# Kernel tuning notes

Hardware: AMD Instinct MI355X
Metric: run time of the kernel (lower is better)

## Reference

```python
import jax, jax.numpy as jnp
import numpy as np

NUM_HEADS = 16
HEAD_DIM = 64
HIDDEN = NUM_HEADS * HEAD_DIM  # 1024
SEQ_LEN = 4096


def setup_inputs() -> dict:
    key = jax.random.key(0)
    ks = jax.random.split(key, 8)
    hidden_states = jax.random.normal(ks[0], (SEQ_LEN, HIDDEN), dtype=jnp.float32)
    cu_seqlens = jnp.sort(jax.random.randint(ks[1], (5,), 0, SEQ_LEN)).astype(jnp.int32)
    cos = jax.random.uniform(ks[2], (SEQ_LEN, HEAD_DIM), dtype=jnp.float32)
    sin = jax.random.uniform(ks[3], (SEQ_LEN, HEAD_DIM), dtype=jnp.float32)
    W_qkv = jax.random.normal(ks[4], (HIDDEN, 3 * HIDDEN), dtype=jnp.float32) * 0.02
    b_qkv = jax.random.normal(ks[5], (3 * HIDDEN,), dtype=jnp.float32) * 0.02
    W_proj = jax.random.normal(ks[6], (HIDDEN, HIDDEN), dtype=jnp.float32) * 0.02
    b_proj = jax.random.normal(ks[7], (HIDDEN,), dtype=jnp.float32) * 0.02
    return {
        "hidden_states": hidden_states,
        "cu_seqlens": cu_seqlens,
        "cos": cos,
        "sin": sin,
        "W_qkv": W_qkv,
        "b_qkv": b_qkv,
        "W_proj": W_proj,
        "b_proj": b_proj,
    }


def _rotate_half(x):
    x1, x2 = jnp.split(x, 2, axis=-1)
    return jnp.concatenate([-x2, x1], axis=-1)


def reference(hidden_states, cu_seqlens, cos, sin, W_qkv, b_qkv, W_proj, b_proj):
    # NOTE: original module does not use cu_seqlens for masking (full dense attention).
    seq_len = hidden_states.shape[0]
    qkv = hidden_states @ W_qkv + b_qkv  # (S, 3*H)
    qkv = qkv.reshape(seq_len, 3, NUM_HEADS, HEAD_DIM)
    q, k, v = qkv[:, 0], qkv[:, 1], qkv[:, 2]  # (S, nh, hd)
    c = cos[:, None, :]
    s = sin[:, None, :]
    q = q * c + _rotate_half(q) * s
    k = k * c + _rotate_half(k) * s
    scale = 1.0 / jnp.sqrt(jnp.float32(HEAD_DIM))
    # (nh, S, hd)
    q = q.transpose(1, 0, 2)
    k = k.transpose(1, 0, 2)
    v = v.transpose(1, 0, 2)
    attn = jnp.einsum('hqd,hkd->hqk', q, k) * scale
    attn = jax.nn.softmax(attn, axis=-1)
    out = jnp.einsum('hqk,hkd->hqd', attn, v)
    out = out.transpose(1, 0, 2).reshape(seq_len, HIDDEN)
    return out @ W_proj + b_proj
```

## Files before the change

kernel.cpp:

```cpp
#include <hip/hip_runtime.h>
#include <type_traits>

typedef short bf16x8 __attribute__((ext_vector_type(8)));
typedef float f32x4  __attribute__((ext_vector_type(4)));
typedef unsigned short u16;

#define MFMA(a,b,c) __builtin_amdgcn_mfma_f32_16x16x32_bf16((a),(b),(c),0,0,0)

__device__ __forceinline__ float bf2f(u16 u){ unsigned x=((unsigned)u)<<16; return __builtin_bit_cast(float,x); }
__device__ __forceinline__ u16 f2bf(float f){ unsigned x=__builtin_bit_cast(unsigned,f); x += 0x7fffu + ((x>>16)&1u); return (u16)(x>>16); }

#if __has_builtin(__builtin_amdgcn_cvt_pk_bf16_f32)
typedef __bf16 hwbf2 __attribute__((ext_vector_type(2)));
__device__ __forceinline__ unsigned pkbf(float a, float b){
  hwbf2 r = __builtin_amdgcn_cvt_pk_bf16_f32(a, b);
  return __builtin_bit_cast(unsigned, r);
}
#else
__device__ __forceinline__ unsigned pkbf(float a, float b){
  unsigned ua = __builtin_bit_cast(unsigned, a), ub = __builtin_bit_cast(unsigned, b);
  ua += 0x7fffu + ((ua>>16)&1u);
  ub += 0x7fffu + ((ub>>16)&1u);
  return __builtin_amdgcn_perm(ub, ua, 0x07060302u);
}
#endif

#if __has_builtin(__builtin_amdgcn_exp2f)
#define EXP2(x) __builtin_amdgcn_exp2f(x)
#else
#define EXP2(x) exp2f(x)
#endif

__device__ __forceinline__ void async_cp16(const u16* g, u16* l){
  __builtin_amdgcn_global_load_lds((const __attribute__((address_space(1))) void*)g,
                                   (__attribute__((address_space(3))) void*)l, 16, 0, 0);
}

__global__ __launch_bounds__(256) void prep(
    const float* __restrict__ H, const float* __restrict__ Wqkv, const float* __restrict__ Wproj,
    u16* __restrict__ Hb, u16* __restrict__ WqkvT, u16* __restrict__ WprojT)
{
  __shared__ u16 tile[32][33];
  const int bid = blockIdx.x, tid = threadIdx.x;
  if (bid < 4096) {
    int i = (bid*256 + tid)*4;
    float4 v = *(const float4*)(H + i);
    ushort4 o;
    o.x = f2bf(v.x); o.y = f2bf(v.y); o.z = f2bf(v.z); o.w = f2bf(v.w);
    *(ushort4*)(Hb + i) = o;
    return;
  }
  const float* in; u16* out; int R, C, bx, by;
  if (bid < 7168) { int t = bid-4096; in=Wqkv; out=WqkvT; R=1024; C=3072; bx=t%96; by=t/96; }
  else            { int t = bid-7168; in=Wproj; out=WprojT; R=1024; C=1024; bx=t%32; by=t/32; }
  int bc = bx*32, br = by*32;
  int tx = tid & 31, ty = tid >> 5;
  #pragma unroll
  for (int i=ty;i<32;i+=8) tile[i][tx] = f2bf(in[(size_t)(br+i)*C + bc + tx]);
  __syncthreads();
  #pragma unroll
  for (int i=ty;i<32;i+=8) out[(size_t)(bc+i)*R + br + tx] = tile[tx][i];
}

__global__ __launch_bounds__(256) void gemm_qkv_rope(
    const u16* __restrict__ A, const u16* __restrict__ Bt,
    const float* __restrict__ bias, const float* __restrict__ cosb, const float* __restrict__ sinb,
    u16* __restrict__ Qo, u16* __restrict__ Ko, u16* __restrict__ Vt)
{
  constexpr int K = 1024;
  __shared__ __align__(16) u16 smem[128*128];
  u16* const As = smem;
  u16* const Bs = smem + 128*64;
  const int m0 = blockIdx.y*128, n0 = blockIdx.x*128;
  const int tid = threadIdx.x, wave = tid>>6, lane = tid&63;
  const int wr = (wave>>1)*64, wc = (wave&1)*64;
  const int ml = lane&15, quad = lane>>4;
  const int lrow8 = lane>>3, lchk = lane&7;
  const int swzg = (lchk ^ lrow8)*8;
  const u16* gA[4]; u16* lA[4];
  const u16* gB[4]; u16* lB[4];
  #pragma unroll
  for (int t=0;t<4;t++){
    gA[t] = A  + (size_t)(m0 + wave*32 + t*8 + lrow8)*K + swzg;
    lA[t] = &As[(wave*32 + t*8)*64];
    gB[t] = Bt + (size_t)(n0 + wave*32 + t*8 + lrow8)*K + swzg;
    lB[t] = &Bs[(wave*32 + t*8)*64];
  }
  f32x4 acc[4][4] = {};
  const int rch0 = ( quad     ^ (ml&7))*8;
  const int rch1 = ((quad|4) ^ (ml&7))*8;
  for (int k0=0; k0<K; k0+=64) {
    #pragma unroll
    for (int t=0;t<4;t++){ async_cp16(gA[t]+k0, lA[t]); async_cp16(gB[t]+k0, lB[t]); }
    __syncthreads();
    #pragma unroll
    for (int kk=0;kk<2;kk++){
      const int rc = kk ? rch1 : rch0;
      bf16x8 af[4], bfr[4];
      #pragma unroll
      for (int i=0;i<4;i++)  af[i]  = *(const bf16x8*)&As[(wr+i*16+ml)*64 + rc];
      #pragma unroll
      for (int j=0;j<4;j++) bfr[j] = *(const bf16x8*)&Bs[(wc+j*16+ml)*64 + rc];
      #pragma unroll
      for (int i=0;i<4;i++)
        #pragma unroll
        for (int j=0;j<4;j++)
          acc[i][j] = MFMA(af[i], bfr[j], acc[i][j]);
    }
    __syncthreads();
  }
  const int region = n0 >> 10;
  if (region == 2) {
    #pragma unroll
    for (int j=0;j<4;j++){
      int d2 = wc + j*16 + ml;
      float bv = bias[n0 + d2];
      #pragma unroll
      for (int i=0;i<4;i++){
        int t0 = wr + i*16 + quad*4;
        #pragma unroll
        for (int r=0;r<4;r++){
          int t = t0 + r;
          int c = (d2 >> 3) ^ (t & 15);
          smem[t*128 + c*8 + (d2 & 7)] = f2bf(acc[i][j][r] + bv);
        }
      }
    }
    __syncthreads();
    const int hbase = (n0 - 2048) >> 6;
    const int pc  = (tid & 15) * 8;
    const int rid = tid >> 4;
    const int tq  = pc >> 5;
    #pragma unroll
    for (int it=0; it<8; it++){
      int d2 = rid + it*16;
      int hh = hbase + (d2 >> 6);
      int dd = d2 & 63;
      union { uint4 u; ushort s[8]; } w;
      #pragma unroll
      for (int pp=0; pp<8; pp++){
        int p = pc + pp;
        int tlog = ((p>>2)&1)*16 + ((p>>3)&3)*4 + (p&3);
        int t_src = tq*32 + tlog;
        int cc = (d2 >> 3) ^ (t_src & 15);
        w.s[pp] = smem[t_src*128 + cc*8 + (d2 & 7)];
      }
      *(uint4*)&Vt[((size_t)hh*64 + dd)*4096 + m0 + pc] = w.u;
    }
  } else {
    u16* dst = region ? Ko : Qo;
    const float qs = region ? 1.0f : 0.125f*1.44269504f;
    #pragma unroll
    for (int j=0;j<4;j++){
      int col = n0 + wc + j*16 + ml;
      int dloc = col & 63, hh = (col & 1023) >> 6;
      float bv  = bias[col];
      float bvp = bias[col ^ 32];
      float sgn = (dloc < 32) ? -1.f : 1.f;
      #pragma unroll
      for (int i=0;i<4;i++){
        int row0 = m0 + wr + i*16 + quad*4;
        #pragma unroll
        for (int r=0;r<4;r++){
          int t = row0 + r;
          float c = cosb[t*64 + dloc], s = sinb[t*64 + dloc];
          float val = acc[i][j][r]   + bv;
          float par = acc[i][j^2][r] + bvp;
          dst[((size_t)hh*4096 + t)*64 + dloc] = f2bf((val*c + sgn*par*s)*qs);
        }
      }
    }
  }
}

template<int BN, typename OutT>
__global__ __launch_bounds__(256) void gemm_bt_bias(
    const u16* __restrict__ A, const u16* __restrict__ Bt,
    const float* __restrict__ bias, OutT* __restrict__ C,
    int M, int N, int K)
{
  __shared__ __align__(16) u16 As[128*64];
  __shared__ __align__(16) u16 Bs[BN*64];
  const int m0 = blockIdx.y*128, n0 = blockIdx.x*BN;
  const int tid = threadIdx.x, wave = tid>>6, lane = tid&63;
  const int wr = (wave>>1)*64, wc = (wave&1)*(BN/2);
  const int ml = lane&15, quad = lane>>4;
  const int lrow8 = lane>>3, lchk = lane&7;
  const int swzg = (lchk ^ lrow8)*8;
  const u16* gA[4]; u16* lA[4];
  #pragma unroll
  for (int t=0;t<4;t++){
    gA[t] = A + (size_t)(m0 + wave*32 + t*8 + lrow8)*K + swzg;
    lA[t] = &As[(wave*32 + t*8)*64];
  }
  constexpr int BI = BN/32;
  const u16* gB[BI]; u16* lB[BI];
  #pragma unroll
  for (int t=0;t<BI;t++){
    gB[t] = Bt + (size_t)(n0 + wave*(BN/4) + t*8 + lrow8)*K + swzg;
    lB[t] = &Bs[(wave*(BN/4) + t*8)*64];
  }
  constexpr int NJ = BN/32;
  f32x4 acc[4][NJ] = {};
  const int rch0 = ( quad     ^ (ml&7))*8;
  const int rch1 = ((quad|4) ^ (ml&7))*8;
  for (int k0=0; k0<K; k0+=64) {
    #pragma unroll
    for (int t=0;t<4;t++)  async_cp16(gA[t]+k0, lA[t]);
    #pragma unroll
    for (int t=0;t<BI;t++) async_cp16(gB[t]+k0, lB[t]);
    __syncthreads();
    #pragma unroll
    for (int kk=0;kk<2;kk++){
      const int rc = kk ? rch1 : rch0;
      bf16x8 af[4], bfr[NJ];
      #pragma unroll
      for (int i=0;i<4;i++)  af[i]  = *(const bf16x8*)&As[(wr+i*16+ml)*64 + rc];
      #pragma unroll
      for (int j=0;j<NJ;j++) bfr[j] = *(const bf16x8*)&Bs[(wc+j*16+ml)*64 + rc];
      #pragma unroll
      for (int i=0;i<4;i++)
        #pragma unroll
        for (int j=0;j<NJ;j++)
          acc[i][j] = MFMA(af[i], bfr[j], acc[i][j]);
    }
    __syncthreads();
  }
  #pragma unroll
  for (int j=0;j<NJ;j++){
    int col = n0 + wc + j*16 + ml;
    float bv = bias[col];
    #pragma unroll
    for (int i=0;i<4;i++){
      int row0 = m0 + wr + i*16 + quad*4;
      #pragma unroll
      for (int r=0;r<4;r++){
        float val = acc[i][j][r] + bv;
        if constexpr (std::is_same_v<OutT, float>)
          C[(size_t)(row0+r)*N + col] = val;
        else
          C[(size_t)(row0+r)*N + col] = f2bf(val);
      }
    }
  }
}

__global__ __launch_bounds__(256,4) void flash_attn(
    const u16* __restrict__ Q, const u16* __restrict__ Kg, const u16* __restrict__ VT,
    u16* __restrict__ O0, u16* __restrict__ O1, float* __restrict__ Lpart)
{
  constexpr int SEQ=4096, HALF=2048;
  __shared__ __align__(16) u16 Ks[64*64];
  __shared__ __align__(16) u16 Vs[64*64];
  const int lin = blockIdx.x;
  const int idx = (lin & 7)*128 + (lin >> 3);
  const int qt = idx & 31, h = (idx >> 5) & 15, ks = idx >> 9;
  const int tid=threadIdx.x, wave=tid>>6, lane=tid&63;
  const int ml=lane&15, quad=lane>>4;
  const int qbase = qt*128 + wave*32;
  bf16x8 qf[2][2];
  #pragma unroll
  for (int qi=0; qi<2; qi++){
    const u16* qp = Q + ((size_t)h*SEQ + qbase + qi*16 + ml)*64;
    qf[qi][0] = *(const bf16x8*)(qp + quad*8);
    qf[qi][1] = *(const bf16x8*)(qp + 32 + quad*8);
  }
  const bf16x8 ones = {0x3F80,0x3F80,0x3F80,0x3F80,0x3F80,0x3F80,0x3F80,0x3F80};
  f32x4 o[2][4] = {};
  f32x4 accsum[2] = {};
  const int lrow8 = lane>>3, lchk = lane&7;
  const int swzg = (lchk ^ lrow8)*8;
  const u16* kgl = Kg + (size_t)h*SEQ*64 + (size_t)(ks*HALF + wave*16 + lrow8)*64 + swzg;
  const u16* vgl = VT + (size_t)h*64*SEQ + (size_t)(wave*16 + lrow8)*SEQ + ks*HALF + swzg;
  u16* kl0 = &Ks[(wave*16  )*64];
  u16* kl1 = &Ks[(wave*16+8)*64];
  u16* vl0 = &Vs[(wave*16  )*64];
  u16* vl1 = &Vs[(wave*16+8)*64];
  const int swzA = ( quad     ^ (ml&7))*8;
  const int swzB = ((quad^4) ^ (ml&7))*8;

  for (int k0=0;k0<HALF;k0+=64) {
    async_cp16(kgl + (size_t)k0*64,       kl0);
    async_cp16(kgl + (size_t)k0*64 + 512, kl1);
    async_cp16(vgl + k0,                  vl0);
    async_cp16(vgl + 8*SEQ + k0,          vl1);
    __syncthreads();
    f32x4 s[2][4];
    #pragma unroll
    for (int kb=0;kb<4;kb++){
      bf16x8 kf0 = *(const bf16x8*)&Ks[(kb*16+ml)*64 + swzA];
      bf16x8 kf1 = *(const bf16x8*)&Ks[(kb*16+ml)*64 + swzB];
      f32x4 z0={0,0,0,0}, z1={0,0,0,0};
      z0 = MFMA(kf0, qf[0][0], z0); s[0][kb] = MFMA(kf1, qf[0][1], z0);
      z1 = MFMA(kf0, qf[1][0], z1); s[1][kb] = MFMA(kf1, qf[1][1], z1);
    }
    bf16x8 vf[4][2];
    #pragma unroll
    for (int db=0;db<4;db++){
      vf[db][0] = *(const bf16x8*)&Vs[(db*16+ml)*64 + swzA];
      vf[db][1] = *(const bf16x8*)&Vs[(db*16+ml)*64 + swzB];
    }
    #pragma unroll
    for (int qi=0; qi<2; qi++)
      #pragma unroll
      for (int p=0;p<2;p++){
        float e0 = EXP2(s[qi][2*p][0]),   e1 = EXP2(s[qi][2*p][1]);
        float e2 = EXP2(s[qi][2*p][2]),   e3 = EXP2(s[qi][2*p][3]);
        float e4 = EXP2(s[qi][2*p+1][0]), e5 = EXP2(s[qi][2*p+1][1]);
        float e6 = EXP2(s[qi][2*p+1][2]), e7 = EXP2(s[qi][2*p+1][3]);
        union { uint4 u; bf16x8 v; } pf;
        pf.u.x = pkbf(e0,e1); pf.u.y = pkbf(e2,e3);
        pf.u.z = pkbf(e4,e5); pf.u.w = pkbf(e6,e7);
        accsum[qi] = MFMA(ones, pf.v, accsum[qi]);
        #pragma unroll
        for (int db=0;db<4;db++)
          o[qi][db] = MFMA(vf[db][p], pf.v, o[qi][db]);
      }
    __syncthreads();
  }
  u16* op = ks ? O1 : O0;
  #pragma unroll
  for (int qi=0;qi<2;qi++){
    size_t rb = (size_t)(qbase + qi*16 + ml)*1024 + h*64;
    #pragma unroll
    for (int db=0;db<4;db++){
      uint2 w;
      w.x = pkbf(o[qi][db][0], o[qi][db][1]);
      w.y = pkbf(o[qi][db][2], o[qi][db][3]);
      *(uint2*)&op[rb + db*16 + quad*4] = w;
    }
  }
  if (quad==0){
    float* lp = Lpart + (size_t)ks*65536 + (size_t)h*4096 + qbase;
    lp[ml]    = accsum[0][0];
    lp[16+ml] = accsum[1][0];
  }
}

__global__ __launch_bounds__(256) void combine_softmax2(
    const u16* __restrict__ O0, const u16* __restrict__ O1,
    const float* __restrict__ L, u16* __restrict__ AO)
{
  int i = (blockIdx.x*256 + threadIdx.x)*4;
  int row = i >> 10, col = i & 1023, h = col >> 6;
  int li = h*4096 + row;
  float inv = 1.f/(L[li] + L[li+65536]);
  ushort4 a = *(const ushort4*)(O0+i);
  ushort4 b = *(const ushort4*)(O1+i);
  ushort4 o;
  o.x = f2bf((bf2f(a.x)+bf2f(b.x))*inv);
  o.y = f2bf((bf2f(a.y)+bf2f(b.y))*inv);
  o.z = f2bf((bf2f(a.z)+bf2f(b.z))*inv);
  o.w = f2bf((bf2f(a.w)+bf2f(b.w))*inv);
  *(ushort4*)(AO+i) = o;
}

extern "C" void kernel_launch(void* const* d_in, const int* in_sizes, int n_in,
                              void* d_out, int out_size, void* d_ws, size_t ws_size,
                              hipStream_t stream)
{
  (void)in_sizes; (void)n_in; (void)out_size; (void)ws_size;
  const float* H     = (const float*)d_in[0];
  const float* cosb  = (const float*)d_in[2];
  const float* sinb  = (const float*)d_in[3];
  const float* Wqkv  = (const float*)d_in[4];
  const float* bqkv  = (const float*)d_in[5];
  const float* Wproj = (const float*)d_in[6];
  const float* bproj = (const float*)d_in[7];
  float* out = (float*)d_out;
  char* ws = (char*)d_ws;
  float* Lpart  = (float*)(ws + 0);
  u16*   WprojT = (u16*)(ws + 2097152);
  u16*   Hb     = (u16*)(ws + 4194304);
  u16*   Opart0 = (u16*)(ws + 4194304);
  u16*   Qb     = (u16*)(ws + 12582912);
  u16*   AO     = (u16*)(ws + 12582912);
  u16*   Kb     = (u16*)(ws + 20971520);
  u16*   VTb    = (u16*)(ws + 29360128);
  u16*   WqkvT  = (u16*)(ws + 37748736);
  u16*   Opart1 = (u16*)(ws + 44040192);

  hipLaunchKernelGGL(prep, dim3(8192), dim3(256), 0, stream, H, Wqkv, Wproj, Hb, WqkvT, WprojT);
  hipLaunchKernelGGL(gemm_qkv_rope, dim3(24,32), dim3(256), 0, stream,
                     Hb, WqkvT, bqkv, cosb, sinb, Qb, Kb, VTb);
  hipLaunchKernelGGL(flash_attn, dim3(1024), dim3(256), 0, stream, Qb, Kb, VTb,
                     Opart0, Opart1, Lpart);
  hipLaunchKernelGGL(combine_softmax2, dim3(4096), dim3(256), 0, stream,
                     Opart0, Opart1, Lpart, AO);
  hipLaunchKernelGGL((gemm_bt_bias<64,float>), dim3(16,32), dim3(256), 0, stream,
                     AO, WprojT, bproj, out, 4096, 1024, 1024);
}
```

Baseline: 237.5 us.

## Fuse split-K softmax combine into output projection GEMM

Removes the separate combine kernel and the AO intermediate buffer. The projection GEMM now loads both partial attention outputs and accumulates MFMAs over each. Because each 64-wide K tile is exactly one head, it scales the per-tile partial sum by the per-row inverse softmax denominator from shared memory. This saves one launch and a full read/write pass of the attention output, but doubles A-tile loads and MFMAs in the projection GEMM and adds LDS use.

Measured after the change: 239.9 us. Within noise of the previous version (+1.0%).

```diff
diff --git a/kernel.cpp b/kernel.cpp
--- a/kernel.cpp
+++ b/kernel.cpp
@@ -168,78 +168,6 @@
           float par = acc[i][j^2][r] + bvp;
           dst[((size_t)hh*4096 + t)*64 + dloc] = f2bf((val*c + sgn*par*s)*qs);
         }
-      }
-    }
-  }
-}
-
-template<int BN, typename OutT>
-__global__ __launch_bounds__(256) void gemm_bt_bias(
-    const u16* __restrict__ A, const u16* __restrict__ Bt,
-    const float* __restrict__ bias, OutT* __restrict__ C,
-    int M, int N, int K)
-{
-  __shared__ __align__(16) u16 As[128*64];
-  __shared__ __align__(16) u16 Bs[BN*64];
-  const int m0 = blockIdx.y*128, n0 = blockIdx.x*BN;
-  const int tid = threadIdx.x, wave = tid>>6, lane = tid&63;
-  const int wr = (wave>>1)*64, wc = (wave&1)*(BN/2);
-  const int ml = lane&15, quad = lane>>4;
-  const int lrow8 = lane>>3, lchk = lane&7;
-  const int swzg = (lchk ^ lrow8)*8;
-  const u16* gA[4]; u16* lA[4];
-  #pragma unroll
-  for (int t=0;t<4;t++){
-    gA[t] = A + (size_t)(m0 + wave*32 + t*8 + lrow8)*K + swzg;
-    lA[t] = &As[(wave*32 + t*8)*64];
-  }
-  constexpr int BI = BN/32;
-  const u16* gB[BI]; u16* lB[BI];
-  #pragma unroll
-  for (int t=0;t<BI;t++){
-    gB[t] = Bt + (size_t)(n0 + wave*(BN/4) + t*8 + lrow8)*K + swzg;
-    lB[t] = &Bs[(wave*(BN/4) + t*8)*64];
-  }
-  constexpr int NJ = BN/32;
-  f32x4 acc[4][NJ] = {};
-  const int rch0 = ( quad     ^ (ml&7))*8;
-  const int rch1 = ((quad|4) ^ (ml&7))*8;
-  for (int k0=0; k0<K; k0+=64) {
-    #pragma unroll
-    for (int t=0;t<4;t++)  async_cp16(gA[t]+k0, lA[t]);
-    #pragma unroll
-    for (int t=0;t<BI;t++) async_cp16(gB[t]+k0, lB[t]);
-    __syncthreads();
-    #pragma unroll
-    for (int kk=0;kk<2;kk++){
-      const int rc = kk ? rch1 : rch0;
-      bf16x8 af[4], bfr[NJ];
-      #pragma unroll
-      for (int i=0;i<4;i++)  af[i]  = *(const bf16x8*)&As[(wr+i*16+ml)*64 + rc];
-      #pragma unroll
-      for (int j=0;j<NJ;j++) bfr[j] = *(const bf16x8*)&Bs[(wc+j*16+ml)*64 + rc];
-      #pragma unroll
-      for (int i=0;i<4;i++)
-        #pragma unroll
-        for (int j=0;j<NJ;j++)
-          acc[i][j] = MFMA(af[i], bfr[j], acc[i][j]);
-    }
-    __syncthreads();
-  }
-  #pragma unroll
-  for (int j=0;j<NJ;j++){
-    int col = n0 + wc + j*16 + ml;
-    float bv = bias[col];
-    #pragma unroll
-    for (int i=0;i<4;i++){
-      int row0 = m0 + wr + i*16 + quad*4;
-      #pragma unroll
-      for (int r=0;r<4;r++){
-        float val = acc[i][j][r] + bv;
-        if constexpr (std::is_same_v<OutT, float>)
-          C[(size_t)(row0+r)*N + col] = val;
-        else
-          C[(size_t)(row0+r)*N + col] = f2bf(val);
       }
     }
   }
@@ -337,22 +265,97 @@
   }
 }
 
-__global__ __launch_bounds__(256) void combine_softmax2(
-    const u16* __restrict__ O0, const u16* __restrict__ O1,
-    const float* __restrict__ L, u16* __restrict__ AO)
-{
-  int i = (blockIdx.x*256 + threadIdx.x)*4;
-  int row = i >> 10, col = i & 1023, h = col >> 6;
-  int li = h*4096 + row;
-  float inv = 1.f/(L[li] + L[li+65536]);
-  ushort4 a = *(const ushort4*)(O0+i);
-  ushort4 b = *(const ushort4*)(O1+i);
-  ushort4 o;
-  o.x = f2bf((bf2f(a.x)+bf2f(b.x))*inv);
-  o.y = f2bf((bf2f(a.y)+bf2f(b.y))*inv);
-  o.z = f2bf((bf2f(a.z)+bf2f(b.z))*inv);
-  o.w = f2bf((bf2f(a.w)+bf2f(b.w))*inv);
-  *(ushort4*)(AO+i) = o;
+__global__ __launch_bounds__(256) void gemm_proj_combine(
+    const u16* __restrict__ O0, const u16* __restrict__ O1, const float* __restrict__ L,
+    const u16* __restrict__ Bt, const float* __restrict__ bias, float* __restrict__ C)
+{
+  constexpr int N = 1024, K = 1024;
+  __shared__ __align__(16) u16 As[128*64];
+  __shared__ __align__(16) u16 A1s[128*64];
+  __shared__ __align__(16) u16 Bs[64*64];
+  __shared__ float invL[16*128];
+  const int m0 = blockIdx.y*128, n0 = blockIdx.x*64;
+  const int tid = threadIdx.x, wave = tid>>6, lane = tid&63;
+  const int wr = (wave>>1)*64, wc = (wave&1)*32;
+  const int ml = lane&15, quad = lane>>4;
+  const int lrow8 = lane>>3, lchk = lane&7;
+  const int swzg = (lchk ^ lrow8)*8;
+  #pragma unroll
+  for (int e = tid; e < 2048; e += 256){
+    int hh = e >> 7, t = e & 127;
+    int li = hh*4096 + m0 + t;
+    invL[e] = 1.0f/(L[li] + L[li + 65536]);
+  }
+  const u16* gA0[4]; u16* lA0[4];
+  const u16* gA1[4]; u16* lA1[4];
+  #pragma unroll
+  for (int t=0;t<4;t++){
+    gA0[t] = O0 + (size_t)(m0 + wave*32 + t*8 + lrow8)*K + swzg;
+    lA0[t] = &As[(wave*32 + t*8)*64];
+    gA1[t] = O1 + (size_t)(m0 + wave*32 + t*8 + lrow8)*K + swzg;
+    lA1[t] = &A1s[(wave*32 + t*8)*64];
+  }
+  const u16* gB[2]; u16* lB[2];
+  #pragma unroll
+  for (int t=0;t<2;t++){
+    gB[t] = Bt + (size_t)(n0 + wave*16 + t*8 + lrow8)*K + swzg;
+    lB[t] = &Bs[(wave*16 + t*8)*64];
+  }
+  f32x4 acc[4][2] = {};
+  const int rch0 = ( quad     ^ (ml&7))*8;
+  const int rch1 = ((quad|4) ^ (ml&7))*8;
+  for (int k0=0; k0<K; k0+=64) {
+    #pragma unroll
+    for (int t=0;t<4;t++){ async_cp16(gA0[t]+k0, lA0[t]); async_cp16(gA1[t]+k0, lA1[t]); }
+    #pragma unroll
+    for (int t=0;t<2;t++)  async_cp16(gB[t]+k0, lB[t]);
+    __syncthreads();
+    f32x4 acch[4][2] = {};
+    #pragma unroll
+    for (int kk=0;kk<2;kk++){
+      const int rc = kk ? rch1 : rch0;
+      bf16x8 af0[4], af1[4], bfr[2];
+      #pragma unroll
+      for (int i=0;i<4;i++){
+        af0[i] = *(const bf16x8*)&As [(wr+i*16+ml)*64 + rc];
+        af1[i] = *(const bf16x8*)&A1s[(wr+i*16+ml)*64 + rc];
+      }
+      #pragma unroll
+      for (int j=0;j<2;j++) bfr[j] = *(const bf16x8*)&Bs[(wc+j*16+ml)*64 + rc];
+      #pragma unroll
+      for (int i=0;i<4;i++)
+        #pragma unroll
+        for (int j=0;j<2;j++){
+          acch[i][j] = MFMA(af0[i], bfr[j], acch[i][j]);
+          acch[i][j] = MFMA(af1[i], bfr[j], acch[i][j]);
+        }
+    }
+    const int h = k0 >> 6;
+    const float* iv = &invL[h*128];
+    #pragma unroll
+    for (int i=0;i<4;i++){
+      #pragma unroll
+      for (int r=0;r<4;r++){
+        float w = iv[wr + i*16 + quad*4 + r];
+        #pragma unroll
+        for (int j=0;j<2;j++)
+          acc[i][j][r] += w * acch[i][j][r];
+      }
+    }
+    __syncthreads();
+  }
+  #pragma unroll
+  for (int j=0;j<2;j++){
+    int col = n0 + wc + j*16 + ml;
+    float bv = bias[col];
+    #pragma unroll
+    for (int i=0;i<4;i++){
+      int row0 = m0 + wr + i*16 + quad*4;
+      #pragma unroll
+      for (int r=0;r<4;r++)
+        C[(size_t)(row0+r)*N + col] = acc[i][j][r] + bv;
+    }
+  }
 }
 
 extern "C" void kernel_launch(void* const* d_in, const int* in_sizes, int n_in,
@@ -374,7 +377,6 @@
   u16*   Hb     = (u16*)(ws + 4194304);
   u16*   Opart0 = (u16*)(ws + 4194304);
   u16*   Qb     = (u16*)(ws + 12582912);
-  u16*   AO     = (u16*)(ws + 12582912);
   u16*   Kb     = (u16*)(ws + 20971520);
   u16*   VTb    = (u16*)(ws + 29360128);
   u16*   WqkvT  = (u16*)(ws + 37748736);
@@ -385,8 +387,6 @@
                      Hb, WqkvT, bqkv, cosb, sinb, Qb, Kb, VTb);
   hipLaunchKernelGGL(flash_attn, dim3(1024), dim3(256), 0, stream, Qb, Kb, VTb,
                      Opart0, Opart1, Lpart);
-  hipLaunchKernelGGL(combine_softmax2, dim3(4096), dim3(256), 0, stream,
-                     Opart0, Opart1, Lpart, AO);
-  hipLaunchKernelGGL((gemm_bt_bias<64,float>), dim3(16,32), dim3(256), 0, stream,
-                     AO, WprojT, bproj, out, 4096, 1024, 1024);
-}
+  hipLaunchKernelGGL(gemm_proj_combine, dim3(16,32), dim3(256), 0, stream,
+                     Opart0, Opart1, Lpart, WprojT, bproj, out);
+}
```
